# Optimization experiments

Measured on AMD Instinct MI355X. Metric: run time of the kernel, lower is better.

## Reference

```python
import jax, jax.numpy as jnp
import numpy as np
from jax import lax

S, B, IN, H, L = 256, 8192, 1, 32, 2


def setup_inputs() -> dict:
    key = jax.random.key(0)
    ks = jax.random.split(key, 12)
    s = 1.0 / np.sqrt(H)
    return {
        "x": jax.random.normal(ks[0], (S, B, IN), dtype=jnp.float32),
        "h": jax.random.normal(ks[1], (L, B, H), dtype=jnp.float32),
        "W_ih0": jax.random.uniform(ks[2], (3 * H, IN), jnp.float32, -s, s),
        "W_hh0": jax.random.uniform(ks[3], (3 * H, H), jnp.float32, -s, s),
        "b_ih0": jax.random.uniform(ks[4], (3 * H,), jnp.float32, -s, s),
        "b_hh0": jax.random.uniform(ks[5], (3 * H,), jnp.float32, -s, s),
        "W_ih1": jax.random.uniform(ks[6], (3 * H, H), jnp.float32, -s, s),
        "W_hh1": jax.random.uniform(ks[7], (3 * H, H), jnp.float32, -s, s),
        "b_ih1": jax.random.uniform(ks[8], (3 * H,), jnp.float32, -s, s),
        "b_hh1": jax.random.uniform(ks[9], (3 * H,), jnp.float32, -s, s),
        "W_out": jax.random.uniform(ks[10], (1, H), jnp.float32, -s, s),
        "b_out": jax.random.uniform(ks[11], (1,), jnp.float32, -s, s),
    }


def _gru_layer(x_seq, h0, W_ih, W_hh, b_ih, b_hh):
    # x_seq: (S, B, D_in), h0: (B, H). PyTorch GRU gate math.
    def step(h, x_t):
        gi = x_t @ W_ih.T + b_ih            # (B, 3H)
        gh = h @ W_hh.T + b_hh              # (B, 3H)
        i_r, i_z, i_n = jnp.split(gi, 3, axis=-1)
        h_r, h_z, h_n = jnp.split(gh, 3, axis=-1)
        r = jax.nn.sigmoid(i_r + h_r)
        z = jax.nn.sigmoid(i_z + h_z)
        n = jnp.tanh(i_n + r * h_n)
        h_new = (1.0 - z) * n + z * h
        return h_new, h_new

    h_last, out = lax.scan(step, h0, x_seq)
    return out, h_last


def reference(x, h, W_ih0, W_hh0, b_ih0, b_hh0, W_ih1, W_hh1, b_ih1, b_hh1, W_out, b_out):
    out0, hl0 = _gru_layer(x, h[0], W_ih0, W_hh0, b_ih0, b_hh0)
    out1, hl1 = _gru_layer(out0, h[1], W_ih1, W_hh1, b_ih1, b_hh1)
    # per-timestep Linear loop == one batched matmul over (S, B, H)
    y = out1 @ W_out.T + b_out              # (S, B, 1)
    h_state = jnp.stack([hl0, hl1], axis=0)  # (L, B, H)
    return (y, h_state)
```

## Files before the change

### kernel.cpp

```cpp
#include <hip/hip_runtime.h>


#define S_LEN 256
#define B_SZ  8192
#define H_SZ  32
#define RS    40

typedef __attribute__((ext_vector_type(8))) short short8;
typedef __attribute__((ext_vector_type(4))) float f32x4;

#define MFMA(a, b, c) __builtin_amdgcn_mfma_f32_16x16x32_bf16(a, b, c, 0, 0, 0)

__device__ __forceinline__ unsigned short bf_rne1(float f) {
    union { float f; unsigned u; } x; x.f = f;
    unsigned u = x.u + 0x7fffu + ((x.u >> 16) & 1u);
    return (unsigned short)(u >> 16);
}

#if __has_builtin(__builtin_amdgcn_cvt_pk_bf16_f32)
typedef __bf16 bf16x2 __attribute__((ext_vector_type(2)));
__device__ __forceinline__ unsigned pk2(float a, float b) {
    union { bf16x2 v; unsigned u; } c;
    c.v = __builtin_amdgcn_cvt_pk_bf16_f32(a, b);
    return c.u;
}
#else
__device__ __forceinline__ unsigned pk2(float a, float b) {
    return (unsigned)bf_rne1(a) | ((unsigned)bf_rne1(b) << 16);
}
#endif

union Frag8 { short8 s8; unsigned u[4]; };

__device__ __forceinline__ uint2 gru_combine(const f32x4& Dr, const f32x4& Dz,
                                             const f32x4& Dn, const f32x4& Dxn,
                                             float* hm) {
    float v4[4];
#pragma unroll
    for (int r = 0; r < 4; ++r) {
        const float Er = __builtin_amdgcn_exp2f(Dr[r]);
        const float rg = __builtin_amdgcn_rcpf(1.0f + Er);
        const float X  = __builtin_amdgcn_exp2f(fmaf(rg, Dn[r], Dxn[r]));
        const float Ez = __builtin_amdgcn_exp2f(Dz[r]);
        const float Nx = 1.0f + X;
        const float Nz = 1.0f + Ez;
        const float P  = Nx * Nz;
        float num = fmaf(-2.0f, Ez, P);
        num = fmaf(hm[r], Nx, num);
        const float v = num * __builtin_amdgcn_rcpf(P);
        hm[r] = v - 1.0f;
        v4[r] = v;
    }
    return make_uint2(pk2(v4[0], v4[1]), pk2(v4[2], v4[3]));
}

__global__ __launch_bounds__(256) void gru_xm(
    const float* __restrict__ x,
    const float* __restrict__ h_in,
    const float* __restrict__ W_ih0,
    const float* __restrict__ W_hh0,
    const float* __restrict__ b_ih0,
    const float* __restrict__ b_hh0,
    const float* __restrict__ W_ih1,
    const float* __restrict__ W_hh1,
    const float* __restrict__ b_ih1,
    const float* __restrict__ b_hh1,
    const float* __restrict__ W_out,
    const float* __restrict__ b_out,
    float* __restrict__ out)
{
    __shared__ __align__(16) unsigned short sh0[2][16 * RS];
    __shared__ __align__(16) unsigned short sh1[2][16 * RS];
    __shared__ __align__(16) float sx[(S_LEN + 1) * 16];
    __shared__ __align__(16) float sy[S_LEN * 16];

    const int tid  = threadIdx.x;
    const int w    = tid >> 6;
    const int lane = tid & 63;
    const int n    = lane & 15;
    const int q    = lane >> 4;
    const int base = blockIdx.x * 16;
    const int bn   = base + n;
    const int wl   = w & 1;

    for (int s = tid; s < S_LEN * 4; s += 256) {
        const int t = s >> 2, c = s & 3;
        *(float4*)&sx[t * 16 + c * 4] = *(const float4*)&x[t * B_SZ + base + c * 4];
    }

    const float SRZ = -1.4426950408889634f;
    const float SN  =  2.8853900817779268f;

    short8 A_h[3], A_i[3];
    f32x4  C_h[3], C_i3;
    short8 Awo = {0, 0, 0, 0, 0, 0, 0, 0};
    short8 Bx  = {0, 0, 0, 0, 0, 0, 0, 0};
    float  hm[4];

    if (w < 2) {
#pragma unroll
        for (int t = 0; t < 3; ++t) {
            const float sc = (t < 2) ? SRZ : SN;
            const int row = 32 * t + 16 * wl + n;
#pragma unroll
            for (int e = 0; e < 8; ++e)
                A_h[t][e] = (short)bf_rne1(W_hh0[row * H_SZ + q * 8 + e] * sc);
#pragma unroll
            for (int e = 0; e < 8; ++e)
                A_i[t][e] = (q == 0 && e == 0)
                            ? (short)bf_rne1(W_ih0[row] * sc) : (short)0;
#pragma unroll
            for (int r = 0; r < 4; ++r) {
                const int g = 32 * t + 16 * wl + 4 * q + r;
                C_h[t][r] = (t < 2) ? SRZ * (b_ih0[g] + b_hh0[g])
                                    : SN * b_hh0[g];
                if (t == 2) C_i3[r] = SN * b_ih0[g];
            }
        }
#pragma unroll
        for (int r = 0; r < 4; ++r)
            hm[r] = h_in[bn * H_SZ + 16 * wl + 4 * q + r] - 1.0f;
    } else {
#pragma unroll
        for (int t = 0; t < 3; ++t) {
            const float sc = (t < 2) ? SRZ : SN;
            const int row = 32 * t + 16 * wl + n;
#pragma unroll
            for (int e = 0; e < 8; ++e) {
                A_h[t][e] = (short)bf_rne1(W_hh1[row * H_SZ + q * 8 + e] * sc);
                A_i[t][e] = (short)bf_rne1(W_ih1[row * H_SZ + q * 8 + e] * sc);
            }
#pragma unroll
            for (int r = 0; r < 4; ++r) {
                const int g = 32 * t + 16 * wl + 4 * q + r;
                C_h[t][r] = (t < 2) ? SRZ * (b_ih1[g] + b_hh1[g])
                                    : SN * b_hh1[g];
                if (t == 2) C_i3[r] = SN * b_ih1[g];
            }
        }
#pragma unroll
        for (int r = 0; r < 4; ++r)
            hm[r] = h_in[B_SZ * H_SZ + bn * H_SZ + 16 * wl + 4 * q + r] - 1.0f;
#pragma unroll
        for (int e = 0; e < 8; ++e)
            Awo[e] = (n == 0) ? (short)bf_rne1(W_out[q * 8 + e]) : (short)0;
    }
    const f32x4 Z4 = {0.f, 0.f, 0.f, 0.f};
    const float bout = b_out[0];

    short8 B0, B1;
    {
        const float* hsrc = h_in + (size_t)(w >= 2) * B_SZ * H_SZ + bn * H_SZ + q * 8;
        Frag8 f;
        const float4 a = *(const float4*)&hsrc[0];
        const float4 b = *(const float4*)&hsrc[4];
        f.u[0] = pk2(a.x, a.y); f.u[1] = pk2(a.z, a.w);
        f.u[2] = pk2(b.x, b.y); f.u[3] = pk2(b.z, b.w);
        if (w < 2) B0 = f.s8; else B1 = f.s8;
    }

    const int wroff = n * RS + 16 * wl + 4 * q;
    const int rdoff = n * RS + 8 * q;

    __syncthreads();
    float xcur = sx[n];
    if (w < 2) __builtin_amdgcn_s_setprio(1);

    if (w < 2) {
        Frag8 bxu; bxu.s8 = Bx; bxu.u[0] = pk2(xcur, xcur); Bx = bxu.s8;
        f32x4 Dr = MFMA(A_h[0], B0, C_h[0]);  Dr = MFMA(A_i[0], Bx, Dr);
        f32x4 Dz = MFMA(A_h[1], B0, C_h[1]);  Dz = MFMA(A_i[1], Bx, Dz);
        f32x4 Dn = MFMA(A_h[2], B0, C_h[2]);
        f32x4 Dxn = MFMA(A_i[2], Bx, C_i3);
        *(uint2*)&sh0[0][wroff] = gru_combine(Dr, Dz, Dn, Dxn, hm);
        xcur = sx[16 + n];
    }
    __syncthreads();
    B0 = *(const short8*)&sh0[0][rdoff];

#pragma unroll 2
    for (int i = 1; i < S_LEN; ++i) {
        const int buf = i & 1;
        if (w < 2) {
            Frag8 bxu; bxu.s8 = Bx; bxu.u[0] = pk2(xcur, xcur); Bx = bxu.s8;
            f32x4 Dr = MFMA(A_h[0], B0, C_h[0]);  Dr = MFMA(A_i[0], Bx, Dr);
            f32x4 Dz = MFMA(A_h[1], B0, C_h[1]);  Dz = MFMA(A_i[1], Bx, Dz);
            f32x4 Dn = MFMA(A_h[2], B0, C_h[2]);
            f32x4 Dxn = MFMA(A_i[2], Bx, C_i3);
            *(uint2*)&sh0[buf][wroff] = gru_combine(Dr, Dz, Dn, Dxn, hm);
            xcur = sx[(i + 1) * 16 + n];
        } else {
            f32x4 Gr = MFMA(A_h[0], B1, C_h[0]);  Gr = MFMA(A_i[0], B0, Gr);
            f32x4 Gz = MFMA(A_h[1], B1, C_h[1]);  Gz = MFMA(A_i[1], B0, Gz);
            f32x4 Un = MFMA(A_h[2], B1, C_h[2]);
            f32x4 Vn = MFMA(A_i[2], B0, C_i3);
            *(uint2*)&sh1[buf][wroff] = gru_combine(Gr, Gz, Un, Vn, hm);
        }

        __syncthreads();

        if (w < 2) {
            B0 = *(const short8*)&sh0[buf][rdoff];
        } else {
            B0 = *(const short8*)&sh0[buf][rdoff];
            B1 = *(const short8*)&sh1[buf][rdoff];
            if (w == 2 + ((i - 1) & 1)) {
                const f32x4 yD = MFMA(Awo, B1, Z4);
                if (lane < 16) sy[(i - 1) * 16 + n] = yD[0];
            }
        }
    }

    if (w >= 2) {
        f32x4 Gr = MFMA(A_h[0], B1, C_h[0]);  Gr = MFMA(A_i[0], B0, Gr);
        f32x4 Gz = MFMA(A_h[1], B1, C_h[1]);  Gz = MFMA(A_i[1], B0, Gz);
        f32x4 Un = MFMA(A_h[2], B1, C_h[2]);
        f32x4 Vn = MFMA(A_i[2], B0, C_i3);
        *(uint2*)&sh1[0][wroff] = gru_combine(Gr, Gz, Un, Vn, hm);
    }
    __syncthreads();
    if (w == 2 + ((S_LEN - 1) & 1)) {
        B1 = *(const short8*)&sh1[0][rdoff];
        const f32x4 yD = MFMA(Awo, B1, Z4);
        if (lane < 16) sy[(S_LEN - 1) * 16 + n] = yD[0];
    }
    __syncthreads();

    for (int s = tid; s < S_LEN * 4; s += 256) {
        const int t = s >> 2, c = s & 3;
        const float4 a = *(const float4*)&sy[t * 16 + c * 4];
        *(float4*)&out[t * B_SZ + base + c * 4] =
            make_float4(a.x + bout, a.y + bout, a.z + bout, a.w + bout);
    }

    const size_t hoff = (size_t)S_LEN * B_SZ + (size_t)(w >= 2) * B_SZ * H_SZ;
    *(float4*)&out[hoff + bn * H_SZ + 16 * wl + 4 * q] =
        make_float4(hm[0] + 1.0f, hm[1] + 1.0f, hm[2] + 1.0f, hm[3] + 1.0f);
}

extern "C" void kernel_launch(void* const* d_in, const int* in_sizes, int n_in,
                              void* d_out, int out_size, void* d_ws, size_t ws_size,
                              hipStream_t stream) {
    (void)in_sizes; (void)n_in; (void)out_size; (void)d_ws; (void)ws_size;
    const float* x     = (const float*)d_in[0];
    const float* h_in  = (const float*)d_in[1];
    const float* W_ih0 = (const float*)d_in[2];
    const float* W_hh0 = (const float*)d_in[3];
    const float* b_ih0 = (const float*)d_in[4];
    const float* b_hh0 = (const float*)d_in[5];
    const float* W_ih1 = (const float*)d_in[6];
    const float* W_hh1 = (const float*)d_in[7];
    const float* b_ih1 = (const float*)d_in[8];
    const float* b_hh1 = (const float*)d_in[9];
    const float* W_out = (const float*)d_in[10];
    const float* b_out = (const float*)d_in[11];

    dim3 grid(B_SZ / 16);
    dim3 block(256);
    gru_xm<<<grid, block, 0, stream>>>(x, h_in, W_ih0, W_hh0, b_ih0, b_hh0,
                                       W_ih1, W_hh1, b_ih1, b_hh1,
                                       W_out, b_out, (float*)d_out);
}
```

Before: 231.1 us.

## Split GRU gate combine across paired waves, doubling block to 512 threads

Each 16x16 gate tile is now processed by two waves instead of one. Both waves issue the same MFMAs, and each applies the sigmoid/tanh combine to only two of the four accumulator rows, halving per-wave transcendental work on the serial recurrence path. The cost is twice the MFMA issue, twice the waves per block, and a larger __syncthreads barrier every timestep. The output-projection MFMA rotates over four layer-1 waves.

```diff
diff --git a/kernel.cpp b/kernel.cpp
--- a/kernel.cpp
+++ b/kernel.cpp
@@ -32,29 +32,43 @@
 
 union Frag8 { short8 s8; unsigned u[4]; };
 
-__device__ __forceinline__ uint2 gru_combine(const f32x4& Dr, const f32x4& Dz,
-                                             const f32x4& Dn, const f32x4& Dxn,
-                                             float* hm) {
-    float v4[4];
-#pragma unroll
-    for (int r = 0; r < 4; ++r) {
-        const float Er = __builtin_amdgcn_exp2f(Dr[r]);
+__device__ __forceinline__ unsigned gru_comb2(const float dr[2], const float dz[2],
+                                              const float dn[2], const float dxn[2],
+                                              float* hm) {
+    float v[2];
+#pragma unroll
+    for (int j = 0; j < 2; ++j) {
+        const float Er = __builtin_amdgcn_exp2f(dr[j]);
         const float rg = __builtin_amdgcn_rcpf(1.0f + Er);
-        const float X  = __builtin_amdgcn_exp2f(fmaf(rg, Dn[r], Dxn[r]));
-        const float Ez = __builtin_amdgcn_exp2f(Dz[r]);
+        const float X  = __builtin_amdgcn_exp2f(fmaf(rg, dn[j], dxn[j]));
+        const float Ez = __builtin_amdgcn_exp2f(dz[j]);
         const float Nx = 1.0f + X;
         const float Nz = 1.0f + Ez;
         const float P  = Nx * Nz;
         float num = fmaf(-2.0f, Ez, P);
-        num = fmaf(hm[r], Nx, num);
-        const float v = num * __builtin_amdgcn_rcpf(P);
-        hm[r] = v - 1.0f;
-        v4[r] = v;
-    }
-    return make_uint2(pk2(v4[0], v4[1]), pk2(v4[2], v4[3]));
-}
-
-__global__ __launch_bounds__(256) void gru_xm(
+        num = fmaf(hm[j], Nx, num);
+        const float vv = num * __builtin_amdgcn_rcpf(P);
+        hm[j] = vv - 1.0f;
+        v[j] = vv;
+    }
+    return pk2(v[0], v[1]);
+}
+
+__device__ __forceinline__ unsigned comb_sel(int sub, const f32x4& Dr, const f32x4& Dz,
+                                             const f32x4& Dn, const f32x4& Dxn,
+                                             float* hm) {
+    if (sub == 0) {
+        const float dr[2]  = {Dr[0], Dr[1]},  dz[2]  = {Dz[0], Dz[1]};
+        const float dn[2]  = {Dn[0], Dn[1]},  dxn[2] = {Dxn[0], Dxn[1]};
+        return gru_comb2(dr, dz, dn, dxn, hm);
+    } else {
+        const float dr[2]  = {Dr[2], Dr[3]},  dz[2]  = {Dz[2], Dz[3]};
+        const float dn[2]  = {Dn[2], Dn[3]},  dxn[2] = {Dxn[2], Dxn[3]};
+        return gru_comb2(dr, dz, dn, dxn, hm);
+    }
+}
+
+__global__ __launch_bounds__(512) void gru_xm(
     const float* __restrict__ x,
     const float* __restrict__ h_in,
     const float* __restrict__ W_ih0,
@@ -76,14 +90,16 @@
 
     const int tid  = threadIdx.x;
     const int w    = tid >> 6;
+    const int sub  = w & 1;
     const int lane = tid & 63;
     const int n    = lane & 15;
     const int q    = lane >> 4;
     const int base = blockIdx.x * 16;
     const int bn   = base + n;
-    const int wl   = w & 1;
-
-    for (int s = tid; s < S_LEN * 4; s += 256) {
+    const int wl   = (w >> 1) & 1;
+    const bool L0  = (w < 4);
+
+    for (int s = tid; s < S_LEN * 4; s += 512) {
         const int t = s >> 2, c = s & 3;
         *(float4*)&sx[t * 16 + c * 4] = *(const float4*)&x[t * B_SZ + base + c * 4];
     }
@@ -95,9 +111,9 @@
     f32x4  C_h[3], C_i3;
     short8 Awo = {0, 0, 0, 0, 0, 0, 0, 0};
     short8 Bx  = {0, 0, 0, 0, 0, 0, 0, 0};
-    float  hm[4];
-
-    if (w < 2) {
+    float  hm[2];
+
+    if (L0) {
 #pragma unroll
         for (int t = 0; t < 3; ++t) {
             const float sc = (t < 2) ? SRZ : SN;
@@ -118,8 +134,8 @@
             }
         }
 #pragma unroll
-        for (int r = 0; r < 4; ++r)
-            hm[r] = h_in[bn * H_SZ + 16 * wl + 4 * q + r] - 1.0f;
+        for (int j = 0; j < 2; ++j)
+            hm[j] = h_in[bn * H_SZ + 16 * wl + 4 * q + 2 * sub + j] - 1.0f;
     } else {
 #pragma unroll
         for (int t = 0; t < 3; ++t) {
@@ -139,8 +155,8 @@
             }
         }
 #pragma unroll
-        for (int r = 0; r < 4; ++r)
-            hm[r] = h_in[B_SZ * H_SZ + bn * H_SZ + 16 * wl + 4 * q + r] - 1.0f;
+        for (int j = 0; j < 2; ++j)
+            hm[j] = h_in[B_SZ * H_SZ + bn * H_SZ + 16 * wl + 4 * q + 2 * sub + j] - 1.0f;
 #pragma unroll
         for (int e = 0; e < 8; ++e)
             Awo[e] = (n == 0) ? (short)bf_rne1(W_out[q * 8 + e]) : (short)0;
@@ -150,29 +166,29 @@
 
     short8 B0, B1;
     {
-        const float* hsrc = h_in + (size_t)(w >= 2) * B_SZ * H_SZ + bn * H_SZ + q * 8;
+        const float* hsrc = h_in + (size_t)(!L0) * B_SZ * H_SZ + bn * H_SZ + q * 8;
         Frag8 f;
         const float4 a = *(const float4*)&hsrc[0];
         const float4 b = *(const float4*)&hsrc[4];
         f.u[0] = pk2(a.x, a.y); f.u[1] = pk2(a.z, a.w);
         f.u[2] = pk2(b.x, b.y); f.u[3] = pk2(b.z, b.w);
-        if (w < 2) B0 = f.s8; else B1 = f.s8;
-    }
-
-    const int wroff = n * RS + 16 * wl + 4 * q;
+        if (L0) B0 = f.s8; else B1 = f.s8;
+    }
+
+    const int wroff = n * RS + 16 * wl + 4 * q + 2 * sub;
     const int rdoff = n * RS + 8 * q;
 
     __syncthreads();
     float xcur = sx[n];
-    if (w < 2) __builtin_amdgcn_s_setprio(1);
-
-    if (w < 2) {
+    if (L0) __builtin_amdgcn_s_setprio(1);
+
+    if (L0) {
         Frag8 bxu; bxu.s8 = Bx; bxu.u[0] = pk2(xcur, xcur); Bx = bxu.s8;
         f32x4 Dr = MFMA(A_h[0], B0, C_h[0]);  Dr = MFMA(A_i[0], Bx, Dr);
         f32x4 Dz = MFMA(A_h[1], B0, C_h[1]);  Dz = MFMA(A_i[1], Bx, Dz);
         f32x4 Dn = MFMA(A_h[2], B0, C_h[2]);
         f32x4 Dxn = MFMA(A_i[2], Bx, C_i3);
-        *(uint2*)&sh0[0][wroff] = gru_combine(Dr, Dz, Dn, Dxn, hm);
+        *(unsigned*)&sh0[0][wroff] = comb_sel(sub, Dr, Dz, Dn, Dxn, hm);
         xcur = sx[16 + n];
     }
     __syncthreads();
@@ -181,61 +197,61 @@
 #pragma unroll 2
     for (int i = 1; i < S_LEN; ++i) {
         const int buf = i & 1;
-        if (w < 2) {
+        if (L0) {
             Frag8 bxu; bxu.s8 = Bx; bxu.u[0] = pk2(xcur, xcur); Bx = bxu.s8;
             f32x4 Dr = MFMA(A_h[0], B0, C_h[0]);  Dr = MFMA(A_i[0], Bx, Dr);
             f32x4 Dz = MFMA(A_h[1], B0, C_h[1]);  Dz = MFMA(A_i[1], Bx, Dz);
             f32x4 Dn = MFMA(A_h[2], B0, C_h[2]);
             f32x4 Dxn = MFMA(A_i[2], Bx, C_i3);
-            *(uint2*)&sh0[buf][wroff] = gru_combine(Dr, Dz, Dn, Dxn, hm);
+            *(unsigned*)&sh0[buf][wroff] = comb_sel(sub, Dr, Dz, Dn, Dxn, hm);
             xcur = sx[(i + 1) * 16 + n];
         } else {
             f32x4 Gr = MFMA(A_h[0], B1, C_h[0]);  Gr = MFMA(A_i[0], B0, Gr);
             f32x4 Gz = MFMA(A_h[1], B1, C_h[1]);  Gz = MFMA(A_i[1], B0, Gz);
             f32x4 Un = MFMA(A_h[2], B1, C_h[2]);
             f32x4 Vn = MFMA(A_i[2], B0, C_i3);
-            *(uint2*)&sh1[buf][wroff] = gru_combine(Gr, Gz, Un, Vn, hm);
+            *(unsigned*)&sh1[buf][wroff] = comb_sel(sub, Gr, Gz, Un, Vn, hm);
         }
 
         __syncthreads();
 
-        if (w < 2) {
+        if (L0) {
             B0 = *(const short8*)&sh0[buf][rdoff];
         } else {
             B0 = *(const short8*)&sh0[buf][rdoff];
             B1 = *(const short8*)&sh1[buf][rdoff];
-            if (w == 2 + ((i - 1) & 1)) {
+            if (w == 4 + ((i - 1) & 3)) {
                 const f32x4 yD = MFMA(Awo, B1, Z4);
                 if (lane < 16) sy[(i - 1) * 16 + n] = yD[0];
             }
         }
     }
 
-    if (w >= 2) {
+    if (!L0) {
         f32x4 Gr = MFMA(A_h[0], B1, C_h[0]);  Gr = MFMA(A_i[0], B0, Gr);
         f32x4 Gz = MFMA(A_h[1], B1, C_h[1]);  Gz = MFMA(A_i[1], B0, Gz);
         f32x4 Un = MFMA(A_h[2], B1, C_h[2]);
         f32x4 Vn = MFMA(A_i[2], B0, C_i3);
-        *(uint2*)&sh1[0][wroff] = gru_combine(Gr, Gz, Un, Vn, hm);
-    }
-    __syncthreads();
-    if (w == 2 + ((S_LEN - 1) & 1)) {
+        *(unsigned*)&sh1[0][wroff] = comb_sel(sub, Gr, Gz, Un, Vn, hm);
+    }
+    __syncthreads();
+    if (w == 4 + ((S_LEN - 1) & 3)) {
         B1 = *(const short8*)&sh1[0][rdoff];
         const f32x4 yD = MFMA(Awo, B1, Z4);
         if (lane < 16) sy[(S_LEN - 1) * 16 + n] = yD[0];
     }
     __syncthreads();
 
-    for (int s = tid; s < S_LEN * 4; s += 256) {
+    for (int s = tid; s < S_LEN * 4; s += 512) {
         const int t = s >> 2, c = s & 3;
         const float4 a = *(const float4*)&sy[t * 16 + c * 4];
         *(float4*)&out[t * B_SZ + base + c * 4] =
             make_float4(a.x + bout, a.y + bout, a.z + bout, a.w + bout);
     }
 
-    const size_t hoff = (size_t)S_LEN * B_SZ + (size_t)(w >= 2) * B_SZ * H_SZ;
-    *(float4*)&out[hoff + bn * H_SZ + 16 * wl + 4 * q] =
-        make_float4(hm[0] + 1.0f, hm[1] + 1.0f, hm[2] + 1.0f, hm[3] + 1.0f);
+    const size_t hoff = (size_t)S_LEN * B_SZ + (size_t)(!L0) * B_SZ * H_SZ;
+    *(float2*)&out[hoff + bn * H_SZ + 16 * wl + 4 * q + 2 * sub] =
+        make_float2(hm[0] + 1.0f, hm[1] + 1.0f);
 }
 
 extern "C" void kernel_launch(void* const* d_in, const int* in_sizes, int n_in,
@@ -256,7 +272,7 @@
     const float* b_out = (const float*)d_in[11];
 
     dim3 grid(B_SZ / 16);
-    dim3 block(256);
+    dim3 block(512);
     gru_xm<<<grid, block, 0, stream>>>(x, h_in, W_ih0, W_hh0, b_ih0, b_hh0,
                                        W_ih1, W_hh1, b_ih1, b_hh1,
                                        W_out, b_out, (float*)d_out);
```

Result: slower. 267.8 us (+15.9%).

## Use one wave per GRU layer with 128-thread blocks instead of two

Applied to the files above, without the earlier changes.

Each layer is now handled by a single wavefront that computes all 32 hidden units, where before two waves each computed 16. This shrinks the block to 128 threads and lets each wave read back its own hidden state from LDS without waiting on the other half. Layer 1 now keeps its state in a single scratch buffer and computes the output projection every step. The cost is twice the MFMA and combine work per wave on the serial critical path, with fewer waves available to hide latency. The s_setprio hint is also removed.

```diff
diff --git a/kernel.cpp b/kernel.cpp
--- a/kernel.cpp
+++ b/kernel.cpp
@@ -54,7 +54,7 @@
     return make_uint2(pk2(v4[0], v4[1]), pk2(v4[2], v4[3]));
 }
 
-__global__ __launch_bounds__(256) void gru_xm(
+__global__ __launch_bounds__(128, 1) void gru_xm(
     const float* __restrict__ x,
     const float* __restrict__ h_in,
     const float* __restrict__ W_ih0,
@@ -69,21 +69,20 @@
     const float* __restrict__ b_out,
     float* __restrict__ out)
 {
-    __shared__ __align__(16) unsigned short sh0[2][16 * RS];
-    __shared__ __align__(16) unsigned short sh1[2][16 * RS];
+    __shared__ __align__(16) unsigned short ring0[2][16 * RS];
+    __shared__ __align__(16) unsigned short scr1[16 * RS];
     __shared__ __align__(16) float sx[(S_LEN + 1) * 16];
     __shared__ __align__(16) float sy[S_LEN * 16];
 
     const int tid  = threadIdx.x;
-    const int w    = tid >> 6;
+    const int role = tid >> 6;
     const int lane = tid & 63;
     const int n    = lane & 15;
     const int q    = lane >> 4;
     const int base = blockIdx.x * 16;
     const int bn   = base + n;
-    const int wl   = w & 1;
-
-    for (int s = tid; s < S_LEN * 4; s += 256) {
+
+    for (int s = tid; s < S_LEN * 4; s += 128) {
         const int t = s >> 2, c = s & 3;
         *(float4*)&sx[t * 16 + c * 4] = *(const float4*)&x[t * B_SZ + base + c * 4];
     }
@@ -91,151 +90,178 @@
     const float SRZ = -1.4426950408889634f;
     const float SN  =  2.8853900817779268f;
 
-    short8 A_h[3], A_i[3];
-    f32x4  C_h[3], C_i3;
+    short8 A_h[6], A_i[6];
+    f32x4  C_h[6], C_i3[2];
     short8 Awo = {0, 0, 0, 0, 0, 0, 0, 0};
     short8 Bx  = {0, 0, 0, 0, 0, 0, 0, 0};
-    float  hm[4];
-
-    if (w < 2) {
+    float  hm0[4], hm1[4];
+
+    if (role == 0) {
 #pragma unroll
         for (int t = 0; t < 3; ++t) {
             const float sc = (t < 2) ? SRZ : SN;
-            const int row = 32 * t + 16 * wl + n;
-#pragma unroll
-            for (int e = 0; e < 8; ++e)
-                A_h[t][e] = (short)bf_rne1(W_hh0[row * H_SZ + q * 8 + e] * sc);
-#pragma unroll
-            for (int e = 0; e < 8; ++e)
-                A_i[t][e] = (q == 0 && e == 0)
-                            ? (short)bf_rne1(W_ih0[row] * sc) : (short)0;
-#pragma unroll
-            for (int r = 0; r < 4; ++r) {
-                const int g = 32 * t + 16 * wl + 4 * q + r;
-                C_h[t][r] = (t < 2) ? SRZ * (b_ih0[g] + b_hh0[g])
-                                    : SN * b_hh0[g];
-                if (t == 2) C_i3[r] = SN * b_ih0[g];
+#pragma unroll
+            for (int m = 0; m < 2; ++m) {
+                const int idx = 2 * t + m;
+                const int row = 32 * t + 16 * m + n;
+#pragma unroll
+                for (int e = 0; e < 8; ++e) {
+                    A_h[idx][e] = (short)bf_rne1(W_hh0[row * H_SZ + q * 8 + e] * sc);
+                    A_i[idx][e] = (q == 0 && e == 0)
+                                  ? (short)bf_rne1(W_ih0[row] * sc) : (short)0;
+                }
+#pragma unroll
+                for (int r = 0; r < 4; ++r) {
+                    const int gr = 32 * t + 16 * m + 4 * q + r;
+                    C_h[idx][r] = (t < 2) ? SRZ * (b_ih0[gr] + b_hh0[gr])
+                                          : SN * b_hh0[gr];
+                    if (t == 2) C_i3[m][r] = SN * b_ih0[gr];
+                }
             }
         }
 #pragma unroll
-        for (int r = 0; r < 4; ++r)
-            hm[r] = h_in[bn * H_SZ + 16 * wl + 4 * q + r] - 1.0f;
+        for (int r = 0; r < 4; ++r) {
+            hm0[r] = h_in[bn * H_SZ + 4 * q + r] - 1.0f;
+            hm1[r] = h_in[bn * H_SZ + 16 + 4 * q + r] - 1.0f;
+        }
     } else {
 #pragma unroll
         for (int t = 0; t < 3; ++t) {
             const float sc = (t < 2) ? SRZ : SN;
-            const int row = 32 * t + 16 * wl + n;
-#pragma unroll
-            for (int e = 0; e < 8; ++e) {
-                A_h[t][e] = (short)bf_rne1(W_hh1[row * H_SZ + q * 8 + e] * sc);
-                A_i[t][e] = (short)bf_rne1(W_ih1[row * H_SZ + q * 8 + e] * sc);
+#pragma unroll
+            for (int m = 0; m < 2; ++m) {
+                const int idx = 2 * t + m;
+                const int row = 32 * t + 16 * m + n;
+#pragma unroll
+                for (int e = 0; e < 8; ++e) {
+                    A_h[idx][e] = (short)bf_rne1(W_hh1[row * H_SZ + q * 8 + e] * sc);
+                    A_i[idx][e] = (short)bf_rne1(W_ih1[row * H_SZ + q * 8 + e] * sc);
+                }
+#pragma unroll
+                for (int r = 0; r < 4; ++r) {
+                    const int gr = 32 * t + 16 * m + 4 * q + r;
+                    C_h[idx][r] = (t < 2) ? SRZ * (b_ih1[gr] + b_hh1[gr])
+                                          : SN * b_hh1[gr];
+                    if (t == 2) C_i3[m][r] = SN * b_ih1[gr];
+                }
             }
-#pragma unroll
-            for (int r = 0; r < 4; ++r) {
-                const int g = 32 * t + 16 * wl + 4 * q + r;
-                C_h[t][r] = (t < 2) ? SRZ * (b_ih1[g] + b_hh1[g])
-                                    : SN * b_hh1[g];
-                if (t == 2) C_i3[r] = SN * b_ih1[g];
-            }
-        }
-#pragma unroll
-        for (int r = 0; r < 4; ++r)
-            hm[r] = h_in[B_SZ * H_SZ + bn * H_SZ + 16 * wl + 4 * q + r] - 1.0f;
+        }
+#pragma unroll
+        for (int r = 0; r < 4; ++r) {
+            hm0[r] = h_in[B_SZ * H_SZ + bn * H_SZ + 4 * q + r] - 1.0f;
+            hm1[r] = h_in[B_SZ * H_SZ + bn * H_SZ + 16 + 4 * q + r] - 1.0f;
+        }
 #pragma unroll
         for (int e = 0; e < 8; ++e)
-            Awo[e] = (n == 0) ? (short)bf_rne1(W_out[q * 8 + e]) : (short)0;
+            Awo[e] = (short)bf_rne1(W_out[q * 8 + e]);
     }
     const f32x4 Z4 = {0.f, 0.f, 0.f, 0.f};
     const float bout = b_out[0];
 
-    short8 B0, B1;
+    short8 Bown;
     {
-        const float* hsrc = h_in + (size_t)(w >= 2) * B_SZ * H_SZ + bn * H_SZ + q * 8;
+        const float* hsrc = h_in + (size_t)role * B_SZ * H_SZ + (size_t)bn * H_SZ + 8 * q;
         Frag8 f;
         const float4 a = *(const float4*)&hsrc[0];
         const float4 b = *(const float4*)&hsrc[4];
         f.u[0] = pk2(a.x, a.y); f.u[1] = pk2(a.z, a.w);
         f.u[2] = pk2(b.x, b.y); f.u[3] = pk2(b.z, b.w);
-        if (w < 2) B0 = f.s8; else B1 = f.s8;
-    }
-
-    const int wroff = n * RS + 16 * wl + 4 * q;
-    const int rdoff = n * RS + 8 * q;
+        Bown = f.s8;
+    }
+
+    const int wr0 = n * RS + 4 * q;
+    const int wr1 = n * RS + 16 + 4 * q;
+    const int rd  = n * RS + 8 * q;
 
     __syncthreads();
-    float xcur = sx[n];
-    if (w < 2) __builtin_amdgcn_s_setprio(1);
-
-    if (w < 2) {
-        Frag8 bxu; bxu.s8 = Bx; bxu.u[0] = pk2(xcur, xcur); Bx = bxu.s8;
-        f32x4 Dr = MFMA(A_h[0], B0, C_h[0]);  Dr = MFMA(A_i[0], Bx, Dr);
-        f32x4 Dz = MFMA(A_h[1], B0, C_h[1]);  Dz = MFMA(A_i[1], Bx, Dz);
-        f32x4 Dn = MFMA(A_h[2], B0, C_h[2]);
-        f32x4 Dxn = MFMA(A_i[2], Bx, C_i3);
-        *(uint2*)&sh0[0][wroff] = gru_combine(Dr, Dz, Dn, Dxn, hm);
-        xcur = sx[16 + n];
+    float xc = sx[n];
+
+    if (role == 0) {
+        Frag8 bxu; bxu.s8 = Bx; bxu.u[0] = pk2(xc, xc); Bx = bxu.s8;
+        f32x4 Dr0 = MFMA(A_h[0], Bown, C_h[0]); Dr0 = MFMA(A_i[0], Bx, Dr0);
+        f32x4 Dr1 = MFMA(A_h[1], Bown, C_h[1]); Dr1 = MFMA(A_i[1], Bx, Dr1);
+        f32x4 Dz0 = MFMA(A_h[2], Bown, C_h[2]); Dz0 = MFMA(A_i[2], Bx, Dz0);
+        f32x4 Dz1 = MFMA(A_h[3], Bown, C_h[3]); Dz1 = MFMA(A_i[3], Bx, Dz1);
+        f32x4 Dn0 = MFMA(A_h[4], Bown, C_h[4]);
+        f32x4 Dn1 = MFMA(A_h[5], Bown, C_h[5]);
+        f32x4 Dx0 = MFMA(A_i[4], Bx, C_i3[0]);
+        f32x4 Dx1 = MFMA(A_i[5], Bx, C_i3[1]);
+        *(uint2*)&ring0[0][wr0] = gru_combine(Dr0, Dz0, Dn0, Dx0, hm0);
+        *(uint2*)&ring0[0][wr1] = gru_combine(Dr1, Dz1, Dn1, Dx1, hm1);
+        Bown = *(const short8*)&ring0[0][rd];
+        xc = sx[16 + n];
     }
     __syncthreads();
-    B0 = *(const short8*)&sh0[0][rdoff];
 
 #pragma unroll 2
     for (int i = 1; i < S_LEN; ++i) {
-        const int buf = i & 1;
-        if (w < 2) {
-            Frag8 bxu; bxu.s8 = Bx; bxu.u[0] = pk2(xcur, xcur); Bx = bxu.s8;
-            f32x4 Dr = MFMA(A_h[0], B0, C_h[0]);  Dr = MFMA(A_i[0], Bx, Dr);
-            f32x4 Dz = MFMA(A_h[1], B0, C_h[1]);  Dz = MFMA(A_i[1], Bx, Dz);
-            f32x4 Dn = MFMA(A_h[2], B0, C_h[2]);
-            f32x4 Dxn = MFMA(A_i[2], Bx, C_i3);
-            *(uint2*)&sh0[buf][wroff] = gru_combine(Dr, Dz, Dn, Dxn, hm);
-            xcur = sx[(i + 1) * 16 + n];
+        if (role == 0) {
+            const int buf = i & 1;
+            Frag8 bxu; bxu.s8 = Bx; bxu.u[0] = pk2(xc, xc); Bx = bxu.s8;
+            f32x4 Dr0 = MFMA(A_h[0], Bown, C_h[0]); Dr0 = MFMA(A_i[0], Bx, Dr0);
+            f32x4 Dr1 = MFMA(A_h[1], Bown, C_h[1]); Dr1 = MFMA(A_i[1], Bx, Dr1);
+            f32x4 Dz0 = MFMA(A_h[2], Bown, C_h[2]); Dz0 = MFMA(A_i[2], Bx, Dz0);
+            f32x4 Dz1 = MFMA(A_h[3], Bown, C_h[3]); Dz1 = MFMA(A_i[3], Bx, Dz1);
+            f32x4 Dn0 = MFMA(A_h[4], Bown, C_h[4]);
+            f32x4 Dn1 = MFMA(A_h[5], Bown, C_h[5]);
+            f32x4 Dx0 = MFMA(A_i[4], Bx, C_i3[0]);
+            f32x4 Dx1 = MFMA(A_i[5], Bx, C_i3[1]);
+            *(uint2*)&ring0[buf][wr0] = gru_combine(Dr0, Dz0, Dn0, Dx0, hm0);
+            *(uint2*)&ring0[buf][wr1] = gru_combine(Dr1, Dz1, Dn1, Dx1, hm1);
+            Bown = *(const short8*)&ring0[buf][rd];
+            xc = sx[(i + 1) * 16 + n];
         } else {
-            f32x4 Gr = MFMA(A_h[0], B1, C_h[0]);  Gr = MFMA(A_i[0], B0, Gr);
-            f32x4 Gz = MFMA(A_h[1], B1, C_h[1]);  Gz = MFMA(A_i[1], B0, Gz);
-            f32x4 Un = MFMA(A_h[2], B1, C_h[2]);
-            f32x4 Vn = MFMA(A_i[2], B0, C_i3);
-            *(uint2*)&sh1[buf][wroff] = gru_combine(Gr, Gz, Un, Vn, hm);
-        }
-
+            const int rb = (i - 1) & 1;
+            const short8 B0p = *(const short8*)&ring0[rb][rd];
+            f32x4 Gr0 = MFMA(A_h[0], Bown, C_h[0]); Gr0 = MFMA(A_i[0], B0p, Gr0);
+            f32x4 Gr1 = MFMA(A_h[1], Bown, C_h[1]); Gr1 = MFMA(A_i[1], B0p, Gr1);
+            f32x4 Gz0 = MFMA(A_h[2], Bown, C_h[2]); Gz0 = MFMA(A_i[2], B0p, Gz0);
+            f32x4 Gz1 = MFMA(A_h[3], Bown, C_h[3]); Gz1 = MFMA(A_i[3], B0p, Gz1);
+            f32x4 Un0 = MFMA(A_h[4], Bown, C_h[4]);
+            f32x4 Un1 = MFMA(A_h[5], Bown, C_h[5]);
+            f32x4 Vn0 = MFMA(A_i[4], B0p, C_i3[0]);
+            f32x4 Vn1 = MFMA(A_i[5], B0p, C_i3[1]);
+            *(uint2*)&scr1[wr0] = gru_combine(Gr0, Gz0, Un0, Vn0, hm0);
+            *(uint2*)&scr1[wr1] = gru_combine(Gr1, Gz1, Un1, Vn1, hm1);
+            Bown = *(const short8*)&scr1[rd];
+            const f32x4 yD = MFMA(Awo, Bown, Z4);
+            if (lane < 16) sy[(i - 1) * 16 + n] = yD[0];
+        }
         __syncthreads();
-
-        if (w < 2) {
-            B0 = *(const short8*)&sh0[buf][rdoff];
-        } else {
-            B0 = *(const short8*)&sh0[buf][rdoff];
-            B1 = *(const short8*)&sh1[buf][rdoff];
-            if (w == 2 + ((i - 1) & 1)) {
-                const f32x4 yD = MFMA(Awo, B1, Z4);
-                if (lane < 16) sy[(i - 1) * 16 + n] = yD[0];
-            }
-        }
-    }
-
-    if (w >= 2) {
-        f32x4 Gr = MFMA(A_h[0], B1, C_h[0]);  Gr = MFMA(A_i[0], B0, Gr);
-        f32x4 Gz = MFMA(A_h[1], B1, C_h[1]);  Gz = MFMA(A_i[1], B0, Gz);
-        f32x4 Un = MFMA(A_h[2], B1, C_h[2]);
-        f32x4 Vn = MFMA(A_i[2], B0, C_i3);
-        *(uint2*)&sh1[0][wroff] = gru_combine(Gr, Gz, Un, Vn, hm);
+    }
+
+    if (role == 1) {
+        const int rb = (S_LEN - 1) & 1;
+        const short8 B0p = *(const short8*)&ring0[rb][rd];
+        f32x4 Gr0 = MFMA(A_h[0], Bown, C_h[0]); Gr0 = MFMA(A_i[0], B0p, Gr0);
+        f32x4 Gr1 = MFMA(A_h[1], Bown, C_h[1]); Gr1 = MFMA(A_i[1], B0p, Gr1);
+        f32x4 Gz0 = MFMA(A_h[2], Bown, C_h[2]); Gz0 = MFMA(A_i[2], B0p, Gz0);
+        f32x4 Gz1 = MFMA(A_h[3], Bown, C_h[3]); Gz1 = MFMA(A_i[3], B0p, Gz1);
+        f32x4 Un0 = MFMA(A_h[4], Bown, C_h[4]);
+        f32x4 Un1 = MFMA(A_h[5], Bown, C_h[5]);
+        f32x4 Vn0 = MFMA(A_i[4], B0p, C_i3[0]);
+        f32x4 Vn1 = MFMA(A_i[5], B0p, C_i3[1]);
+        *(uint2*)&scr1[wr0] = gru_combine(Gr0, Gz0, Un0, Vn0, hm0);
+        *(uint2*)&scr1[wr1] = gru_combine(Gr1, Gz1, Un1, Vn1, hm1);
+        Bown = *(const short8*)&scr1[rd];
+        const f32x4 yD = MFMA(Awo, Bown, Z4);
+        if (lane < 16) sy[(S_LEN - 1) * 16 + n] = yD[0];
     }
     __syncthreads();
-    if (w == 2 + ((S_LEN - 1) & 1)) {
-        B1 = *(const short8*)&sh1[0][rdoff];
-        const f32x4 yD = MFMA(Awo, B1, Z4);
-        if (lane < 16) sy[(S_LEN - 1) * 16 + n] = yD[0];
-    }
-    __syncthreads();
-
-    for (int s = tid; s < S_LEN * 4; s += 256) {
+
+    for (int s = tid; s < S_LEN * 4; s += 128) {
         const int t = s >> 2, c = s & 3;
         const float4 a = *(const float4*)&sy[t * 16 + c * 4];
         *(float4*)&out[t * B_SZ + base + c * 4] =
             make_float4(a.x + bout, a.y + bout, a.z + bout, a.w + bout);
     }
 
-    const size_t hoff = (size_t)S_LEN * B_SZ + (size_t)(w >= 2) * B_SZ * H_SZ;
-    *(float4*)&out[hoff + bn * H_SZ + 16 * wl + 4 * q] =
-        make_float4(hm[0] + 1.0f, hm[1] + 1.0f, hm[2] + 1.0f, hm[3] + 1.0f);
+    const size_t hoff = (size_t)S_LEN * B_SZ + (size_t)role * B_SZ * H_SZ
+                      + (size_t)bn * H_SZ;
+    *(float4*)&out[hoff + 4 * q] =
+        make_float4(hm0[0] + 1.0f, hm0[1] + 1.0f, hm0[2] + 1.0f, hm0[3] + 1.0f);
+    *(float4*)&out[hoff + 16 + 4 * q] =
+        make_float4(hm1[0] + 1.0f, hm1[1] + 1.0f, hm1[2] + 1.0f, hm1[3] + 1.0f);
 }
 
 extern "C" void kernel_launch(void* const* d_in, const int* in_sizes, int n_in,
@@ -256,7 +282,7 @@
     const float* b_out = (const float*)d_in[11];
 
     dim3 grid(B_SZ / 16);
-    dim3 block(256);
+    dim3 block(128);
     gru_xm<<<grid, block, 0, stream>>>(x, h_in, W_ih0, W_hh0, b_ih0, b_hh0,
                                        W_ih1, W_hh1, b_ih1, b_hh1,
                                        W_out, b_out, (float*)d_out);
```

Result: slower. 347.9 us (+50.5%).

## Precompute input-gate MFMAs before the barrier and stagger block start times

Applied to the files above, without the earlier changes.

The input-projection MFMAs (x for layer 0, layer-0 output for layer 1) now run for the next step right after the barrier, before the next step begins. Their results are passed as accumulators into the recurrent MFMAs, which shortens the dependent MFMA chain on the serial critical path of each step. Odd blocks also sleep briefly at startup to desynchronise phases across blocks sharing a CU. The cost is extra live accumulator registers and a small startup delay.

```diff
diff --git a/kernel.cpp b/kernel.cpp
--- a/kernel.cpp
+++ b/kernel.cpp
@@ -93,6 +93,7 @@
 
     short8 A_h[3], A_i[3];
     f32x4  C_h[3], C_i3;
+    f32x4  Pr, Pz, Pn;
     short8 Awo = {0, 0, 0, 0, 0, 0, 0, 0};
     short8 Bx  = {0, 0, 0, 0, 0, 0, 0, 0};
     float  hm[4];
@@ -163,44 +164,63 @@
     const int rdoff = n * RS + 8 * q;
 
     __syncthreads();
+
+    if ((blockIdx.x ^ (blockIdx.x >> 8)) & 1) __builtin_amdgcn_s_sleep(12);
+
     float xcur = sx[n];
     if (w < 2) __builtin_amdgcn_s_setprio(1);
 
     if (w < 2) {
         Frag8 bxu; bxu.s8 = Bx; bxu.u[0] = pk2(xcur, xcur); Bx = bxu.s8;
-        f32x4 Dr = MFMA(A_h[0], B0, C_h[0]);  Dr = MFMA(A_i[0], Bx, Dr);
-        f32x4 Dz = MFMA(A_h[1], B0, C_h[1]);  Dz = MFMA(A_i[1], Bx, Dz);
+        Pr = MFMA(A_i[0], Bx, C_h[0]);
+        Pz = MFMA(A_i[1], Bx, C_h[1]);
+        Pn = MFMA(A_i[2], Bx, C_i3);
+    }
+
+    if (w < 2) {
+        f32x4 Dr = MFMA(A_h[0], B0, Pr);
+        f32x4 Dz = MFMA(A_h[1], B0, Pz);
         f32x4 Dn = MFMA(A_h[2], B0, C_h[2]);
-        f32x4 Dxn = MFMA(A_i[2], Bx, C_i3);
-        *(uint2*)&sh0[0][wroff] = gru_combine(Dr, Dz, Dn, Dxn, hm);
+        *(uint2*)&sh0[0][wroff] = gru_combine(Dr, Dz, Dn, Pn, hm);
         xcur = sx[16 + n];
     }
     __syncthreads();
     B0 = *(const short8*)&sh0[0][rdoff];
+    if (w < 2) {
+        Frag8 bxu; bxu.s8 = Bx; bxu.u[0] = pk2(xcur, xcur); Bx = bxu.s8;
+        Pr = MFMA(A_i[0], Bx, C_h[0]);
+        Pz = MFMA(A_i[1], Bx, C_h[1]);
+        Pn = MFMA(A_i[2], Bx, C_i3);
+    } else {
+        Pr = MFMA(A_i[0], B0, C_h[0]);
+        Pz = MFMA(A_i[1], B0, C_h[1]);
+        Pn = MFMA(A_i[2], B0, C_i3);
+    }
 
 #pragma unroll 2
     for (int i = 1; i < S_LEN; ++i) {
         const int buf = i & 1;
         if (w < 2) {
-            Frag8 bxu; bxu.s8 = Bx; bxu.u[0] = pk2(xcur, xcur); Bx = bxu.s8;
-            f32x4 Dr = MFMA(A_h[0], B0, C_h[0]);  Dr = MFMA(A_i[0], Bx, Dr);
-            f32x4 Dz = MFMA(A_h[1], B0, C_h[1]);  Dz = MFMA(A_i[1], Bx, Dz);
+            f32x4 Dr = MFMA(A_h[0], B0, Pr);
+            f32x4 Dz = MFMA(A_h[1], B0, Pz);
             f32x4 Dn = MFMA(A_h[2], B0, C_h[2]);
-            f32x4 Dxn = MFMA(A_i[2], Bx, C_i3);
-            *(uint2*)&sh0[buf][wroff] = gru_combine(Dr, Dz, Dn, Dxn, hm);
+            *(uint2*)&sh0[buf][wroff] = gru_combine(Dr, Dz, Dn, Pn, hm);
             xcur = sx[(i + 1) * 16 + n];
         } else {
-            f32x4 Gr = MFMA(A_h[0], B1, C_h[0]);  Gr = MFMA(A_i[0], B0, Gr);
-            f32x4 Gz = MFMA(A_h[1], B1, C_h[1]);  Gz = MFMA(A_i[1], B0, Gz);
+            f32x4 Gr = MFMA(A_h[0], B1, Pr);
+            f32x4 Gz = MFMA(A_h[1], B1, Pz);
             f32x4 Un = MFMA(A_h[2], B1, C_h[2]);
-            f32x4 Vn = MFMA(A_i[2], B0, C_i3);
-            *(uint2*)&sh1[buf][wroff] = gru_combine(Gr, Gz, Un, Vn, hm);
+            *(uint2*)&sh1[buf][wroff] = gru_combine(Gr, Gz, Un, Pn, hm);
         }
 
         __syncthreads();
 
         if (w < 2) {
             B0 = *(const short8*)&sh0[buf][rdoff];
+            Frag8 bxu; bxu.s8 = Bx; bxu.u[0] = pk2(xcur, xcur); Bx = bxu.s8;
+            Pr = MFMA(A_i[0], Bx, C_h[0]);
+            Pz = MFMA(A_i[1], Bx, C_h[1]);
+            Pn = MFMA(A_i[2], Bx, C_i3);
         } else {
             B0 = *(const short8*)&sh0[buf][rdoff];
             B1 = *(const short8*)&sh1[buf][rdoff];
@@ -208,15 +228,17 @@
                 const f32x4 yD = MFMA(Awo, B1, Z4);
                 if (lane < 16) sy[(i - 1) * 16 + n] = yD[0];
             }
+            Pr = MFMA(A_i[0], B0, C_h[0]);
+            Pz = MFMA(A_i[1], B0, C_h[1]);
+            Pn = MFMA(A_i[2], B0, C_i3);
         }
     }
 
     if (w >= 2) {
-        f32x4 Gr = MFMA(A_h[0], B1, C_h[0]);  Gr = MFMA(A_i[0], B0, Gr);
-        f32x4 Gz = MFMA(A_h[1], B1, C_h[1]);  Gz = MFMA(A_i[1], B0, Gz);
+        f32x4 Gr = MFMA(A_h[0], B1, Pr);
+        f32x4 Gz = MFMA(A_h[1], B1, Pz);
         f32x4 Un = MFMA(A_h[2], B1, C_h[2]);
-        f32x4 Vn = MFMA(A_i[2], B0, C_i3);
-        *(uint2*)&sh1[0][wroff] = gru_combine(Gr, Gz, Un, Vn, hm);
+        *(uint2*)&sh1[0][wroff] = gru_combine(Gr, Gz, Un, Pn, hm);
     }
     __syncthreads();
     if (w == 2 + ((S_LEN - 1) & 1)) {
```

New measurement: 237.9 us. 2.9% more time.
